# Kernel optimization log

Measured on AMD Instinct MI355X. Metric: run time of the kernel, lower is better.

Reference implementation:

```python
import jax, jax.numpy as jnp
import numpy as np
from jax import lax

R = 1.0                 # object_bounding_sphere
SDF_THR = 5e-05
LINE_SEARCH_STEP = 0.5
LINE_STEP_ITERS = 1
SPHERE_TRACING_ITERS = 10
N_STEPS = 100
N_SECANT = 8
B, P = 4, 32768


def _sdf(p, center, radius):
    # analytic sphere SDF standing in for the opaque external sdf network
    return jnp.sqrt(jnp.sum((p - center) ** 2, axis=-1) + 1e-12) - radius[0]


def setup_inputs() -> dict:
    key = jax.random.key(0)
    k1, k2, k3 = jax.random.split(key, 3)
    cd = jax.random.normal(k1, (B, 3), dtype=jnp.float32)
    cam_loc = 2.5 * cd / jnp.linalg.norm(cd, axis=-1, keepdims=True)  # cameras outside bounding sphere
    d = -cam_loc[:, None, :] + 0.5 * jax.random.normal(k2, (B, P, 3), dtype=jnp.float32)
    ray_directions = d / jnp.linalg.norm(d, axis=-1, keepdims=True)   # rays aimed near origin
    object_mask = jax.random.bernoulli(k3, 0.5, (B * P,))
    sdf_center = jnp.array([0.1, -0.05, 0.08], dtype=jnp.float32)
    sdf_radius = jnp.array([0.7], dtype=jnp.float32)
    return {"cam_loc": cam_loc, "ray_directions": ray_directions,
            "object_mask": object_mask, "sdf_center": sdf_center, "sdf_radius": sdf_radius}


def _safe_div(a, b):
    return a / jnp.where(b == 0, 1.0, b)


def _forward(cam_loc, ray_directions, sdf_center, sdf_radius):
    sdf = lambda p: _sdf(p, sdf_center, sdf_radius)
    b, p, _ = ray_directions.shape
    n = b * p
    dirs = ray_directions.reshape(n, 3)
    cam = jnp.broadcast_to(cam_loc[:, None, :], (b, p, 3)).reshape(n, 3)

    # ---- sphere intersection with bounding sphere of radius R ----
    ray_cam_dot = jnp.einsum('nd,nd->n', dirs, cam)
    under_sqrt = ray_cam_dot ** 2 - (jnp.sum(cam ** 2, axis=-1) - R ** 2)
    mask_intersect = under_sqrt > 0
    sq = jnp.sqrt(jnp.where(mask_intersect, under_sqrt, 0.0))
    si = jnp.stack([-sq - ray_cam_dot, sq - ray_cam_dot], axis=-1)   # [N,2] near/far distances
    si = jnp.maximum(jnp.where(mask_intersect[:, None], si, 0.0), 0.0)

    # ---- sphere tracing (fixed trip count; masked lanes are no-ops, matching the torch early-break) ----
    acc_s = jnp.where(mask_intersect, si[:, 0], 0.0)
    acc_e = jnp.where(mask_intersect, si[:, 1], 0.0)
    pts_s = jnp.where(mask_intersect[:, None], cam + acc_s[:, None] * dirs, 0.0)
    pts_e = jnp.where(mask_intersect[:, None], cam + acc_e[:, None] * dirs, 0.0)
    next_s = jnp.where(mask_intersect, sdf(pts_s), 0.0)
    next_e = jnp.where(mask_intersect, sdf(pts_e), 0.0)

    def body(i, st):
        unfin_s, unfin_e, acc_s, acc_e, next_s, next_e, pts_s, pts_e = st
        curr_s = jnp.where(unfin_s, next_s, 0.0)
        curr_s = jnp.where(curr_s <= SDF_THR, 0.0, curr_s)
        curr_e = jnp.where(unfin_e, next_e, 0.0)
        curr_e = jnp.where(curr_e <= SDF_THR, 0.0, curr_e)
        unfin_s = unfin_s & (curr_s > SDF_THR)
        unfin_e = unfin_e & (curr_e > SDF_THR)
        acc_s = acc_s + curr_s
        acc_e = acc_e - curr_e
        pts_s = cam + acc_s[:, None] * dirs
        pts_e = cam + acc_e[:, None] * dirs
        next_s = jnp.where(unfin_s, sdf(pts_s), 0.0)
        next_e = jnp.where(unfin_e, sdf(pts_e), 0.0)
        # line search back-off for overshoot (line_step_iters fixed small)
        for j in range(LINE_STEP_ITERS):
            step = (1.0 - LINE_SEARCH_STEP) / (2.0 ** j)
            np_s = next_s < 0
            np_e = next_e < 0
            acc_s = jnp.where(np_s, acc_s - step * curr_s, acc_s)
            acc_e = jnp.where(np_e, acc_e + step * curr_e, acc_e)
            pts_s = jnp.where(np_s[:, None], cam + acc_s[:, None] * dirs, pts_s)
            pts_e = jnp.where(np_e[:, None], cam + acc_e[:, None] * dirs, pts_e)
            next_s = jnp.where(np_s, sdf(pts_s), next_s)
            next_e = jnp.where(np_e, sdf(pts_e), next_e)
        ok = acc_s < acc_e
        return (unfin_s & ok, unfin_e & ok, acc_s, acc_e, next_s, next_e, pts_s, pts_e)

    st = (mask_intersect, mask_intersect, acc_s, acc_e, next_s, next_e, pts_s, pts_e)
    unfin_s, unfin_e, acc_s, acc_e, next_s, next_e, pts_s, pts_e = lax.fori_loop(
        0, SPHERE_TRACING_ITERS, body, st)
    # final mask refresh (the break iteration of the torch while-loop)
    curr_s = jnp.where(unfin_s, next_s, 0.0)
    curr_s = jnp.where(curr_s <= SDF_THR, 0.0, curr_s)
    unfin_s = unfin_s & (curr_s > SDF_THR)

    network_object_mask = acc_s < acc_e
    sampler_mask = unfin_s

    # ---- ray sampler: dense march along unconverged rays ----
    smin = jnp.where(sampler_mask, acc_s, 0.0)
    smax = jnp.where(sampler_mask, acc_e, 0.0)
    t = jnp.linspace(0.0, 1.0, N_STEPS)
    z = smin[:, None] + t[None, :] * (smax - smin)[:, None]          # [N,S]
    pts = cam[:, None, :] + z[..., None] * dirs[:, None, :]          # [N,S,3]
    sdf_val = sdf(pts)                                               # [N,S]
    # first index where sign flips to negative (IDR trick)
    tmp = jnp.sign(sdf_val) * jnp.arange(N_STEPS, 0, -1, dtype=sdf_val.dtype)
    ind = jnp.argmin(tmp, axis=-1)
    row = jnp.arange(n)
    z_high = z[row, ind]
    sdf_high = sdf_val[row, ind]
    p_ind = pts[row, ind]
    net_surface = sdf_high < 0
    z_low = z[row, ind - 1]      # ind==0 wraps, same as torch -1 indexing
    sdf_low = sdf_val[row, ind - 1]

    # ---- secant root finding ----
    z_pred = -sdf_low * _safe_div(z_high - z_low, sdf_high - sdf_low) + z_low

    def sec_body(i, st):
        z_low, z_high, sdf_low, sdf_high, z_pred = st
        sdf_mid = sdf(cam + z_pred[:, None] * dirs)
        low_m = sdf_mid > 0
        high_m = sdf_mid < 0
        z_low = jnp.where(low_m, z_pred, z_low)
        sdf_low = jnp.where(low_m, sdf_mid, sdf_low)
        z_high = jnp.where(high_m, z_pred, z_high)
        sdf_high = jnp.where(high_m, sdf_mid, sdf_high)
        z_pred = -sdf_low * _safe_div(z_high - z_low, sdf_high - sdf_low) + z_low
        return (z_low, z_high, sdf_low, sdf_high, z_pred)

    _, _, _, _, z_pred = lax.fori_loop(0, N_SECANT, sec_body,
                                       (z_low, z_high, sdf_low, sdf_high, z_pred))

    secant_mask = sampler_mask & net_surface
    sampler_pts = jnp.where(secant_mask[:, None], cam + z_pred[:, None] * dirs, p_ind)
    sampler_dists = jnp.where(secant_mask, z_pred, z_high)
    sampler_net_obj_mask = sampler_mask & net_surface

    curr_start_points = jnp.where(sampler_mask[:, None], sampler_pts, pts_s)
    acc_start_dis = jnp.where(sampler_mask, sampler_dists, acc_s)
    network_object_mask = jnp.where(sampler_mask, sampler_net_obj_mask, network_object_mask)
    return curr_start_points, network_object_mask, acc_start_dis


def reference(cam_loc, ray_directions, object_mask, sdf_center, sdf_radius):
    # eval-mode forward: object_mask only affects the training-only tail of torch forward
    return _forward(cam_loc, ray_directions, sdf_center, sdf_radius)
```

## Files before the change

kernel.cpp:

```cpp
#include <hip/hip_runtime.h>


#define SDF_THR   5e-05f
#define NSTEPS    100
#define NTRACE    10

__device__ __forceinline__ float fsqrt(float x) {
    float r; asm("v_sqrt_f32 %0, %1" : "=v"(r) : "v"(x)); return r;
}
__device__ __forceinline__ float frcp(float x) {
    float r; asm("v_rcp_f32 %0, %1" : "=v"(r) : "v"(x)); return r;
}
__device__ __forceinline__ float dpp_xor1(float x) {
    return __int_as_float(__builtin_amdgcn_update_dpp(
        0, __float_as_int(x), 0xB1, 0xF, 0xF, true));
}
__device__ __forceinline__ int dpp_xor1_i(int x) {
    return __builtin_amdgcn_update_dpp(0, x, 0xB1, 0xF, 0xF, true);
}

__global__ __launch_bounds__(256) void ray_kernel(
    const float* __restrict__ cam_loc,
    const float* __restrict__ ray_dirs,
    const float* __restrict__ sdf_center,
    const float* __restrict__ sdf_radius,
    float* __restrict__ out,
    int n_total)
{
    const int t = blockIdx.x * blockDim.x + threadIdx.x;
    const int n = t >> 1;
    const int h = t & 1;
    if (n >= n_total) return;
    const int b = n >> 15;

    const float dx = ray_dirs[3*n+0], dy = ray_dirs[3*n+1], dz = ray_dirs[3*n+2];
    const float cx = cam_loc[3*b+0], cy = cam_loc[3*b+1], cz = cam_loc[3*b+2];
    const float scx = sdf_center[0], scy = sdf_center[1], scz = sdf_center[2];
    const float rad = sdf_radius[0];

    const float r2 = rad * rad;
    unsigned rb = __float_as_uint(r2);
    float u_neg_max = __uint_as_float(rb - 7u);
    float u_le_max  = u_neg_max;
    #pragma unroll
    for (int k = -6; k <= 6; ++k) {
        float u = __uint_as_float(rb + (unsigned)k);
        float v = fsqrt(u);
        if (v <  rad) u_neg_max = u;
        if (v <= rad) u_le_max  = u;
    }

    const float ex = cx - scx, ey = cy - scy, ez = cz - scz;
    const float dd  = dx*dx + dy*dy + dz*dz;
    const float de2 = 2.0f * (dx*ex + dy*ey + dz*ez);
    const float ee1 = (ex*ex + ey*ey + ez*ez) + 1e-12f;

    float rcd  = dx*cx + dy*cy + dz*cz;
    float cam2 = cx*cx + cy*cy + cz*cz;
    float under = rcd*rcd - (cam2 - 1.0f);
    bool mask_int = under > 0.0f;
    float sq = fsqrt(mask_int ? under : 0.0f);
    float si0 = fmaxf(mask_int ? (-sq - rcd) : 0.0f, 0.0f);
    float si1 = fmaxf(mask_int ? ( sq - rcd) : 0.0f, 0.0f);

    float my_acc = h ? si1 : si0;
    const float sgn = h ? -1.0f : 1.0f;
    bool my_unfin = mask_int;
    float next;
    {
        float u0 = fmaf(my_acc, fmaf(my_acc, dd, de2), ee1);
        next = my_unfin ? (fsqrt(u0) - rad) : 0.0f;
    }

    float acc_s = my_acc, acc_e = my_acc;
    #pragma unroll
    for (int it = 0; it < NTRACE; ++it) {
        float curr = my_unfin ? next : 0.0f;
        curr = (curr <= SDF_THR) ? 0.0f : curr;
        my_unfin = my_unfin && (curr > SDF_THR);
        my_acc = fmaf(sgn, curr, my_acc);
        float u = fmaf(my_acc, fmaf(my_acc, dd, de2), ee1);
        next = my_unfin ? (fsqrt(u) - rad) : 0.0f;
        if (next < 0.0f) {
            my_acc = fmaf(-sgn, 0.5f * curr, my_acc);
            float u2 = fmaf(my_acc, fmaf(my_acc, dd, de2), ee1);
            next = fsqrt(u2) - rad;
        }
        float pacc = dpp_xor1(my_acc);
        acc_s = h ? pacc : my_acc;
        acc_e = h ? my_acc : pacc;
        bool ok = acc_s < acc_e;
        my_unfin = my_unfin && ok;
    }
    bool sampler_s = my_unfin;
    {
        float curr = my_unfin ? next : 0.0f;
        curr = (curr <= SDF_THR) ? 0.0f : curr;
        sampler_s = my_unfin && (curr > SDF_THR);
    }
    const bool netmask_trace = acc_s < acc_e;

    int fs = h ? 0 : (int)sampler_s;
    int other = dpp_xor1_i(fs);
    const bool sampler = h ? (other != 0) : sampler_s;

    bool net_surface = false;
    float z_pred = 0.0f, zh_out = 0.0f;
    float pix = 0.0f, piy = 0.0f, piz = 0.0f;

    if (__ballot(sampler) != 0ULL) {
        const float smin = sampler ? acc_s : 0.0f;
        const float smax = sampler ? acc_e : 0.0f;
        const float sz = (smax - smin) * (1.0f / 99.0f);

        float kmf = 1e30f;
        float i_f = (float)h;
        #pragma unroll
        for (int s = 0; s < NSTEPS / 2; ++s) {
            float z = fmaf(i_f, sz, smin);
            float u = fmaf(z, fmaf(z, dd, de2), ee1);
            kmf = fminf(kmf, (u <= u_le_max) ? i_f : 1e30f);
            i_f += 2.0f;
        }
        kmf = fminf(kmf, dpp_xor1(kmf));

        int ind;
        if (kmf < 1e29f) {
            int km = (int)kmf;
            float zk = fmaf(kmf, sz, smin);
            float uk = fmaf(zk, fmaf(zk, dd, de2), ee1);
            if (uk <= u_neg_max) {
                ind = km; net_surface = true;
            } else {
                ind = km; net_surface = false;
                for (int i = km + 1; i < NSTEPS; ++i) {
                    float z = fmaf((float)i, sz, smin);
                    float u = fmaf(z, fmaf(z, dd, de2), ee1);
                    if (u <= u_neg_max) { ind = i; net_surface = true; break; }
                }
            }
        } else {
            ind = NSTEPS - 1; net_surface = false;
        }

        zh_out = fmaf((float)ind, sz, smin);
        pix = fmaf(zh_out, dx, cx);
        piy = fmaf(zh_out, dy, cy);
        piz = fmaf(zh_out, dz, cz);

        float Bh = 0.5f * de2;
        float disc2 = fmaf(-dd, ee1 - r2, Bh * Bh);
        z_pred = (-Bh - fsqrt(fmaxf(disc2, 0.0f))) * frcp(dd);
    }

    float ox, oy, oz, odis;
    bool omask;
    if (sampler) {
        if (net_surface) {
            ox = fmaf(z_pred, dx, cx);
            oy = fmaf(z_pred, dy, cy);
            oz = fmaf(z_pred, dz, cz);
            odis = z_pred;
        } else {
            ox = pix; oy = piy; oz = piz;
            odis = zh_out;
        }
        omask = net_surface;
    } else {
        ox = fmaf(acc_s, dx, cx);
        oy = fmaf(acc_s, dy, cy);
        oz = fmaf(acc_s, dz, cz);
        odis = acc_s;
        omask = netmask_trace;
    }

    if (h == 0) {
        out[3*n + 0] = ox;
        out[3*n + 1] = oy;
        out[3*n + 2] = oz;
    } else {
        out[3*n_total + n] = omask ? 1.0f : 0.0f;
        out[4*n_total + n] = odis;
    }
}

extern "C" void kernel_launch(void* const* d_in, const int* in_sizes, int n_in,
                              void* d_out, int out_size, void* d_ws, size_t ws_size,
                              hipStream_t stream) {
    const float* cam_loc    = (const float*)d_in[0];
    const float* ray_dirs   = (const float*)d_in[1];
    const float* sdf_center = (const float*)d_in[3];
    const float* sdf_radius = (const float*)d_in[4];
    float* out = (float*)d_out;

    int n_total = in_sizes[1] / 3;
    int threads = 2 * n_total;
    int block = 256;
    int grid = (threads + block - 1) / block;
    ray_kernel<<<grid, block, 0, stream>>>(cam_loc, ray_dirs, sdf_center,
                                           sdf_radius, out, n_total);
}
```

Measured before the change: 11.13 us.

## Process both trace directions per thread instead of splitting rays across lane pairs

Each ray now runs on a single thread that performs start- and end-point sphere tracing together, removing the two-lanes-per-ray split and its DPP exchanges. The 100-step sampler scan is done fully by one thread with partial unrolling rather than interleaved across two lanes. This halves the thread count and removes redundant per-lane setup and cross-lane shuffles, at the cost of more serial work and registers per thread and less available parallelism.

```diff
diff --git a/kernel.cpp b/kernel.cpp
--- a/kernel.cpp
+++ b/kernel.cpp
@@ -11,13 +11,6 @@
 __device__ __forceinline__ float frcp(float x) {
     float r; asm("v_rcp_f32 %0, %1" : "=v"(r) : "v"(x)); return r;
 }
-__device__ __forceinline__ float dpp_xor1(float x) {
-    return __int_as_float(__builtin_amdgcn_update_dpp(
-        0, __float_as_int(x), 0xB1, 0xF, 0xF, true));
-}
-__device__ __forceinline__ int dpp_xor1_i(int x) {
-    return __builtin_amdgcn_update_dpp(0, x, 0xB1, 0xF, 0xF, true);
-}
 
 __global__ __launch_bounds__(256) void ray_kernel(
     const float* __restrict__ cam_loc,
@@ -27,9 +20,7 @@
     float* __restrict__ out,
     int n_total)
 {
-    const int t = blockIdx.x * blockDim.x + threadIdx.x;
-    const int n = t >> 1;
-    const int h = t & 1;
+    const int n = blockIdx.x * blockDim.x + threadIdx.x;
     if (n >= n_total) return;
     const int b = n >> 15;
 
@@ -63,46 +54,51 @@
     float si0 = fmaxf(mask_int ? (-sq - rcd) : 0.0f, 0.0f);
     float si1 = fmaxf(mask_int ? ( sq - rcd) : 0.0f, 0.0f);
 
-    float my_acc = h ? si1 : si0;
-    const float sgn = h ? -1.0f : 1.0f;
-    bool my_unfin = mask_int;
-    float next;
+    float acc_s = si0, acc_e = si1;
+    bool unfin_s = mask_int, unfin_e = mask_int;
+    float next_s, next_e;
     {
-        float u0 = fmaf(my_acc, fmaf(my_acc, dd, de2), ee1);
-        next = my_unfin ? (fsqrt(u0) - rad) : 0.0f;
+        float us = fmaf(acc_s, fmaf(acc_s, dd, de2), ee1);
+        float ue = fmaf(acc_e, fmaf(acc_e, dd, de2), ee1);
+        next_s = unfin_s ? (fsqrt(us) - rad) : 0.0f;
+        next_e = unfin_e ? (fsqrt(ue) - rad) : 0.0f;
     }
 
-    float acc_s = my_acc, acc_e = my_acc;
     #pragma unroll
     for (int it = 0; it < NTRACE; ++it) {
-        float curr = my_unfin ? next : 0.0f;
-        curr = (curr <= SDF_THR) ? 0.0f : curr;
-        my_unfin = my_unfin && (curr > SDF_THR);
-        my_acc = fmaf(sgn, curr, my_acc);
-        float u = fmaf(my_acc, fmaf(my_acc, dd, de2), ee1);
-        next = my_unfin ? (fsqrt(u) - rad) : 0.0f;
-        if (next < 0.0f) {
-            my_acc = fmaf(-sgn, 0.5f * curr, my_acc);
-            float u2 = fmaf(my_acc, fmaf(my_acc, dd, de2), ee1);
-            next = fsqrt(u2) - rad;
+        float curr_s = unfin_s ? next_s : 0.0f;
+        curr_s = (curr_s <= SDF_THR) ? 0.0f : curr_s;
+        float curr_e = unfin_e ? next_e : 0.0f;
+        curr_e = (curr_e <= SDF_THR) ? 0.0f : curr_e;
+        unfin_s = unfin_s && (curr_s > SDF_THR);
+        unfin_e = unfin_e && (curr_e > SDF_THR);
+        acc_s = acc_s + curr_s;
+        acc_e = acc_e - curr_e;
+        float us = fmaf(acc_s, fmaf(acc_s, dd, de2), ee1);
+        float ue = fmaf(acc_e, fmaf(acc_e, dd, de2), ee1);
+        next_s = unfin_s ? (fsqrt(us) - rad) : 0.0f;
+        next_e = unfin_e ? (fsqrt(ue) - rad) : 0.0f;
+        if (next_s < 0.0f) {
+            acc_s = fmaf(-0.5f, curr_s, acc_s);
+            float u2 = fmaf(acc_s, fmaf(acc_s, dd, de2), ee1);
+            next_s = fsqrt(u2) - rad;
         }
-        float pacc = dpp_xor1(my_acc);
-        acc_s = h ? pacc : my_acc;
-        acc_e = h ? my_acc : pacc;
+        if (next_e < 0.0f) {
+            acc_e = fmaf(0.5f, curr_e, acc_e);
+            float u2 = fmaf(acc_e, fmaf(acc_e, dd, de2), ee1);
+            next_e = fsqrt(u2) - rad;
+        }
         bool ok = acc_s < acc_e;
-        my_unfin = my_unfin && ok;
+        unfin_s = unfin_s && ok;
+        unfin_e = unfin_e && ok;
     }
-    bool sampler_s = my_unfin;
+    bool sampler = unfin_s;
     {
-        float curr = my_unfin ? next : 0.0f;
-        curr = (curr <= SDF_THR) ? 0.0f : curr;
-        sampler_s = my_unfin && (curr > SDF_THR);
+        float curr_s = unfin_s ? next_s : 0.0f;
+        curr_s = (curr_s <= SDF_THR) ? 0.0f : curr_s;
+        sampler = unfin_s && (curr_s > SDF_THR);
     }
     const bool netmask_trace = acc_s < acc_e;
-
-    int fs = h ? 0 : (int)sampler_s;
-    int other = dpp_xor1_i(fs);
-    const bool sampler = h ? (other != 0) : sampler_s;
 
     bool net_surface = false;
     float z_pred = 0.0f, zh_out = 0.0f;
@@ -114,15 +110,14 @@
         const float sz = (smax - smin) * (1.0f / 99.0f);
 
         float kmf = 1e30f;
-        float i_f = (float)h;
-        #pragma unroll
-        for (int s = 0; s < NSTEPS / 2; ++s) {
+        float i_f = 0.0f;
+        #pragma unroll 4
+        for (int s = 0; s < NSTEPS; ++s) {
             float z = fmaf(i_f, sz, smin);
             float u = fmaf(z, fmaf(z, dd, de2), ee1);
             kmf = fminf(kmf, (u <= u_le_max) ? i_f : 1e30f);
-            i_f += 2.0f;
+            i_f += 1.0f;
         }
-        kmf = fminf(kmf, dpp_xor1(kmf));
 
         int ind;
         if (kmf < 1e29f) {
@@ -174,14 +169,11 @@
         omask = netmask_trace;
     }
 
-    if (h == 0) {
-        out[3*n + 0] = ox;
-        out[3*n + 1] = oy;
-        out[3*n + 2] = oz;
-    } else {
-        out[3*n_total + n] = omask ? 1.0f : 0.0f;
-        out[4*n_total + n] = odis;
-    }
+    out[3*n + 0] = ox;
+    out[3*n + 1] = oy;
+    out[3*n + 2] = oz;
+    out[3*n_total + n] = omask ? 1.0f : 0.0f;
+    out[4*n_total + n] = odis;
 }
 
 extern "C" void kernel_launch(void* const* d_in, const int* in_sizes, int n_in,
@@ -194,9 +186,8 @@
     float* out = (float*)d_out;
 
     int n_total = in_sizes[1] / 3;
-    int threads = 2 * n_total;
     int block = 256;
-    int grid = (threads + block - 1) / block;
+    int grid = (n_total + block - 1) / block;
     ray_kernel<<<grid, block, 0, stream>>>(cam_loc, ray_dirs, sdf_center,
                                            sdf_radius, out, n_total);
 }
```

Measured after the change: 11.73 us. 1.05x slower.
